# Optimization experiments

Measured on AMD Instinct MI355X. Metric: run time of the kernel, lower is better.

The kernel has to match this reference:

```python
import jax, jax.numpy as jnp
import numpy as np

N_NODES = 100000
N_EDGES = 1200000
D_IN = 64
D_OUT = 32
BN_EPS = 1e-5


def setup_inputs() -> dict:
    key = jax.random.key(0)
    ks = jax.random.split(key, 8)
    x = jax.random.normal(ks[0], (N_NODES, D_IN), dtype=jnp.float32)
    edge_index = jax.random.randint(ks[1], (2, N_EDGES), 0, N_NODES, dtype=jnp.int64)
    W1s = jax.random.normal(ks[2], (3, D_IN, D_IN), dtype=jnp.float32) * 0.05
    b1s = jax.random.normal(ks[3], (3, D_IN), dtype=jnp.float32) * 0.05
    W2s = jax.random.normal(ks[4], (3, D_IN, D_IN), dtype=jnp.float32) * 0.05
    b2s = jax.random.normal(ks[5], (3, D_IN), dtype=jnp.float32) * 0.05
    gammas = jnp.ones((3, D_IN), dtype=jnp.float32)
    betas = jnp.zeros((3, D_IN), dtype=jnp.float32)
    epss = jnp.zeros((3,), dtype=jnp.float32)  # GINConv train_eps init value 0
    lin_w = jax.random.normal(ks[6], (D_IN, D_OUT), dtype=jnp.float32) * 0.05
    lin_b = jnp.zeros((D_OUT,), dtype=jnp.float32)
    return {"x": x, "edge_index": edge_index, "W1s": W1s, "b1s": b1s,
            "W2s": W2s, "b2s": b2s, "gammas": gammas, "betas": betas,
            "epss": epss, "lin_w": lin_w, "lin_b": lin_b}


def reference(x, edge_index, W1s, b1s, W2s, b2s, gammas, betas, epss, lin_w, lin_b):
    # PyG GINConv (source_to_target): out_i = nn((1+eps)*x_i + sum_{j->i} x_j)
    src = edge_index[0]
    dst = edge_index[1]
    n = x.shape[0]
    h = x
    for i in range(3):
        agg = jax.ops.segment_sum(h[src], dst, num_segments=n)  # [N, d]
        z = (1.0 + epss[i]) * h + agg
        z = jax.nn.relu(z @ W1s[i] + b1s[i])
        z = jax.nn.relu(z @ W2s[i] + b2s[i])
        # BatchNorm1d, training mode (batch statistics, biased variance)
        mu = jnp.mean(z, axis=0)
        var = jnp.var(z, axis=0)
        z = gammas[i] * (z - mu) * jax.lax.rsqrt(var + BN_EPS) + betas[i]
        h = jax.nn.relu(z)  # F.relu after each conv
    return h @ lin_w + lin_b  # [N, D_OUT]
```

## Files before the change

### kernel.cpp

```cpp
#include <hip/hip_runtime.h>
#include <hip/hip_fp16.h>

#define NBMAX 256
#define BCAP  8192
#define CHB   3584

typedef _Float16 half8 __attribute__((ext_vector_type(8)));
typedef float f32x4 __attribute__((ext_vector_type(4)));

__device__ __forceinline__ unsigned short f2h(float f) {
    __half h = __float2half_rn(f);
    return *(unsigned short*)&h;
}

__device__ __forceinline__ int scan256(int v, int* wsum, int* woff) {
    int t = threadIdx.x, lane = t & 63, wv = t >> 6;
    int x = v;
    #pragma unroll
    for (int d = 1; d < 64; d <<= 1) {
        int y = __shfl_up(x, d, 64);
        if (lane >= d) x += y;
    }
    if (lane == 63) wsum[wv] = x;
    __syncthreads();
    if (t == 0) {
        int a = 0;
        #pragma unroll
        for (int i = 0; i < 4; ++i) { woff[i] = a; a += wsum[i]; }
    }
    __syncthreads();
    return x - v + woff[wv];
}

__global__ __launch_bounds__(256) void gin_prep(const float* __restrict__ x,
                                                unsigned short* __restrict__ o, int n16,
                                                const void* __restrict__ edge,
                                                int* __restrict__ gcount,
                                                uint2* __restrict__ ebuf,
                                                int E, int nb, int nbin) {
    if ((int)blockIdx.x >= nbin) {
        int i = (blockIdx.x - nbin) * 256 + threadIdx.x;
        if (i >= n16) return;
        float4 v = ((const float4*)x)[i];
        ushort4 u;
        u.x = f2h(v.x); u.y = f2h(v.y); u.z = f2h(v.z); u.w = f2h(v.w);
        ((ushort4*)o)[i] = u;
        return;
    }
    __shared__ int cnt[NBMAX];
    __shared__ int dlt[NBMAX];
    __shared__ int cur[NBMAX];
    __shared__ int wsum[4], woff[4];
    __shared__ int s_is64;
    __shared__ uint2 buf[CHB];
    int t = threadIdx.x;
    int beg = blockIdx.x * CHB;
    int m = E - beg; if (m > CHB) m = CHB;
    if (t < nb) cnt[t] = 0;
    if (t == 0) s_is64 = 1;
    __syncthreads();
    {
        int m2 = (E < 64) ? E : 64;
        if (t < m2 && ((const int*)edge)[2 * t + 1] != 0) s_is64 = 0;
    }
    __syncthreads();
    int is64 = s_is64;
    for (int j = t; j < m; j += 256) {
        int e = beg + j;
        int d = is64 ? (int)((const long long*)edge)[E + e] : ((const int*)edge)[E + e];
        atomicAdd(&cnt[d >> 9], 1);
    }
    __syncthreads();
    int v = (t < nb) ? cnt[t] : 0;
    int excl = scan256(v, wsum, woff);
    if (t < nb) {
        int gb = v ? atomicAdd(&gcount[t], v) : 0;
        dlt[t] = t * BCAP + gb - excl;
        cur[t] = excl;
    }
    __syncthreads();
    for (int j = t; j < m; j += 256) {
        int e = beg + j;
        int s, d;
        if (is64) {
            s = (int)((const long long*)edge)[e];
            d = (int)((const long long*)edge)[E + e];
        } else {
            s = ((const int*)edge)[e];
            d = ((const int*)edge)[E + e];
        }
        int p = atomicAdd(&cur[d >> 9], 1);
        buf[p] = make_uint2((unsigned)s, (unsigned)d);
    }
    __syncthreads();
    for (int j = t; j < m; j += 256) {
        uint2 ed = buf[j];
        ebuf[j + dlt[(int)(ed.y >> 9)]] = ed;
    }
}

__global__ __launch_bounds__(256) void gin_build(const uint2* __restrict__ ebuf,
                                                 const int* __restrict__ gcount,
                                                 int* __restrict__ rowbeg,
                                                 int* __restrict__ rowend,
                                                 int* __restrict__ col, int n) {
    __shared__ int cnt[512];
    __shared__ int off[512];
    __shared__ int wsum[4], woff[4];
    int b = blockIdx.x, t = threadIdx.x;
    int beg = b * BCAP;
    int end = beg + gcount[b];
    cnt[t] = 0; cnt[t + 256] = 0;
    __syncthreads();
    for (int j = beg + t; j < end; j += 256)
        atomicAdd(&cnt[(int)(ebuf[j].y & 511)], 1);
    __syncthreads();
    int v0 = cnt[2 * t], v1 = cnt[2 * t + 1];
    int ep = scan256(v0 + v1, wsum, woff);
    off[2 * t] = ep;
    off[2 * t + 1] = ep + v0;
    __syncthreads();
    int node0 = b * 512 + 2 * t;
    if (node0 < n) {
        rowbeg[node0] = beg + off[2 * t];
        rowend[node0] = beg + off[2 * t] + v0;
    }
    if (node0 + 1 < n) {
        rowbeg[node0 + 1] = beg + off[2 * t + 1];
        rowend[node0 + 1] = beg + off[2 * t + 1] + v1;
    }
    __syncthreads();
    for (int j = beg + t; j < end; j += 256) {
        uint2 ed = ebuf[j];
        int p = atomicAdd(&off[(int)(ed.y & 511)], 1);
        col[beg + p] = (int)ed.x;
    }
}

template <bool APPLY>
__device__ __forceinline__ void accum8(float* acc, uint4 u,
                                       const float* sc, const float* sh) {
    float v[8];
    float2 f;
    f = __half22float2(*(const __half2*)&u.x); v[0] = f.x; v[1] = f.y;
    f = __half22float2(*(const __half2*)&u.y); v[2] = f.x; v[3] = f.y;
    f = __half22float2(*(const __half2*)&u.z); v[4] = f.x; v[5] = f.y;
    f = __half22float2(*(const __half2*)&u.w); v[6] = f.x; v[7] = f.y;
    #pragma unroll
    for (int j = 0; j < 8; ++j)
        acc[j] += APPLY ? fmaxf(fmaf(v[j], sc[j], sh[j]), 0.f) : v[j];
}

template <bool APPLY>
__device__ __forceinline__ void gather_node(const unsigned short* __restrict__ zb,
                                            int r0, int r1, int ci0,
                                            const int* __restrict__ col,
                                            float e1,
                                            const float* sc, const float* sh,
                                            _Float16* __restrict__ trow,
                                            int wid, int qn, int l16) {
    int r = l16 >> 3, c = l16 & 7;
    uint4 su = make_uint4(0, 0, 0, 0);
    if (r == 0) su = *(const uint4*)(zb + (size_t)wid * 64 + 8 * c);

    float acc[8] = {0.f, 0.f, 0.f, 0.f, 0.f, 0.f, 0.f, 0.f};
    int ci = ci0;
    for (int b2 = r0; b2 < r1; b2 += 16) {
        if (b2 > r0) {
            int ce = b2 + l16;
            ci = col[ce < r1 ? ce : r1 - 1];
        }
        uint4 u[8];
        bool p[8];
        #pragma unroll
        for (int s = 0; s < 8; ++s) {
            int j = 2 * s + r;
            p[s] = (b2 + j) < r1;
            int idx = __shfl(ci, 16 * qn + j);
            if (p[s]) u[s] = *(const uint4*)(zb + (size_t)idx * 64 + 8 * c);
        }
        #pragma unroll
        for (int s = 0; s < 8; ++s)
            if (p[s]) accum8<APPLY>(acc, u[s], sc, sh);
    }
    #pragma unroll
    for (int j = 0; j < 8; ++j)
        acc[j] += __shfl_xor(acc[j], 8);
    if (r == 0) {
        float s[8];
        float2 f;
        f = __half22float2(*(const __half2*)&su.x); s[0] = f.x; s[1] = f.y;
        f = __half22float2(*(const __half2*)&su.y); s[2] = f.x; s[3] = f.y;
        f = __half22float2(*(const __half2*)&su.z); s[4] = f.x; s[5] = f.y;
        f = __half22float2(*(const __half2*)&su.w); s[6] = f.x; s[7] = f.y;
        #pragma unroll
        for (int j = 0; j < 8; ++j) {
            float v = APPLY ? fmaxf(fmaf(s[j], sc[j], sh[j]), 0.f) : s[j];
            acc[j] = fmaf(e1, v, acc[j]);
        }
        uint4 o;
        o.x = (unsigned)f2h(acc[0]) | ((unsigned)f2h(acc[1]) << 16);
        o.y = (unsigned)f2h(acc[2]) | ((unsigned)f2h(acc[3]) << 16);
        o.z = (unsigned)f2h(acc[4]) | ((unsigned)f2h(acc[5]) << 16);
        o.w = (unsigned)f2h(acc[6]) | ((unsigned)f2h(acc[7]) << 16);
        *(uint4*)(trow + 8 * c) = o;
    }
}

template <bool APPLY>
__global__ __launch_bounds__(512, 4) void gin_fused(const unsigned short* __restrict__ zb,
                                                    const int* __restrict__ rowbeg,
                                                    const int* __restrict__ rowend,
                                                    const int* __restrict__ col,
                                                    const float* __restrict__ epss,
                                                    const float* __restrict__ gammas,
                                                    const float* __restrict__ betas,
                                                    float fN,
                                                    unsigned short* __restrict__ z16,
                                                    const float* __restrict__ W1g,
                                                    const float* __restrict__ b1g,
                                                    const float* __restrict__ W2g,
                                                    const float* __restrict__ b2g,
                                                    float* __restrict__ stats,
                                                    int layer, int n) {
    __shared__ _Float16 Wt[2 * 64 * 72];
    __shared__ _Float16 Tz[128 * 72];
    __shared__ float sS[64], sQ[64];
    __shared__ float sBN[128];
    int tid = threadIdx.x;
    int base = blockIdx.x * 128;
    const float* __restrict__ W1 = W1g + layer * 4096;
    const float* __restrict__ W2 = W2g + layer * 4096;

    for (int i = tid; i < 4096; i += 512) {
        int k = i >> 6, nn = i & 63;
        Wt[nn * 72 + k]        = (_Float16)W1[i];
        Wt[4608 + nn * 72 + k] = (_Float16)W2[i];
    }
    if (tid < 64) {
        sS[tid] = 0.f; sQ[tid] = 0.f;
        if (APPLY) {
            float mu  = stats[(layer - 1) * 128 + tid] / fN;
            float var = stats[(layer - 1) * 128 + 64 + tid] / fN - mu * mu;
            float g   = gammas[(layer - 1) * 64 + tid];
            float grs = g * rsqrtf(var + 1e-5f);
            sBN[tid]      = grs;
            sBN[64 + tid] = betas[(layer - 1) * 64 + tid] - grs * mu;
        }
    }
    __syncthreads();

    int lane = tid & 63, wv = tid >> 6;
    int qn = lane >> 4;
    int l16 = lane & 15;
    int c8 = l16 & 7;
    float e1 = 1.f + epss[layer];
    float sc[8] = {1.f, 1.f, 1.f, 1.f, 1.f, 1.f, 1.f, 1.f};
    float sh[8] = {0.f, 0.f, 0.f, 0.f, 0.f, 0.f, 0.f, 0.f};
    if (APPLY) {
        *(float4*)&sc[0] = *(const float4*)&sBN[8 * c8];
        *(float4*)&sc[4] = *(const float4*)&sBN[8 * c8 + 4];
        *(float4*)&sh[0] = *(const float4*)&sBN[64 + 8 * c8];
        *(float4*)&sh[4] = *(const float4*)&sBN[64 + 8 * c8 + 4];
    }

    int wvq = wv * 4 + qn;
    int cr0, cr1, pr0, pr1;
    {
        int w0 = base + wvq;
        cr0 = 0; cr1 = 0;
        if (w0 < n) { cr0 = rowbeg[w0]; cr1 = rowend[w0]; }
        int w1 = w0 + 32;
        pr0 = 0; pr1 = 0;
        if (w1 < n) { pr0 = rowbeg[w1]; pr1 = rowend[w1]; }
    }
    int cci = 0;
    if (cr1 > cr0) { int ce = cr0 + l16; cci = col[ce < cr1 ? ce : cr1 - 1]; }
    #pragma unroll 1
    for (int p = 0; p < 4; ++p) {
        int nci = 0;
        if (pr1 > pr0) { int ce = pr0 + l16; nci = col[ce < pr1 ? ce : pr1 - 1]; }
        int fr0 = 0, fr1 = 0;
        {
            int w2 = base + (p + 2) * 32 + wvq;
            if (p < 2 && w2 < n) { fr0 = rowbeg[w2]; fr1 = rowend[w2]; }
        }
        int widl = p * 32 + wvq;
        int wid = base + widl;
        if (wid < n) {
            gather_node<APPLY>(zb, cr0, cr1, cci, col, e1, sc, sh,
                               Tz + widl * 72, wid, qn, l16);
        } else if (l16 < 8) {
            *(uint4*)(Tz + widl * 72 + 8 * c8) = make_uint4(0u, 0u, 0u, 0u);
        }
        cr0 = pr0; cr1 = pr1; cci = nci;
        pr0 = fr0; pr1 = fr1;
    }
    __syncthreads();

    int g = qn, q = l16;
    int n0 = 16 * wv + q;

    half8 tb0 = *(const half8*)&Tz[n0 * 72 + 8 * g];
    half8 tb1 = *(const half8*)&Tz[n0 * 72 + 32 + 8 * g];

    f32x4 acc[4];
    #pragma unroll
    for (int ft = 0; ft < 4; ++ft)
        acc[ft] = (f32x4){0.f, 0.f, 0.f, 0.f};

    #pragma unroll
    for (int ft = 0; ft < 4; ++ft) {
        half8 a0 = *(const half8*)&Wt[(16 * ft + q) * 72 + 8 * g];
        half8 a1 = *(const half8*)&Wt[(16 * ft + q) * 72 + 32 + 8 * g];
        acc[ft] = __builtin_amdgcn_mfma_f32_16x16x32_f16(a0, tb0, acc[ft], 0, 0, 0);
        acc[ft] = __builtin_amdgcn_mfma_f32_16x16x32_f16(a1, tb1, acc[ft], 0, 0, 0);
    }

    #pragma unroll
    for (int ft = 0; ft < 4; ++ft) {
        float4 b = *(const float4*)(b1g + layer * 64 + 16 * ft + 4 * g);
        float v0 = fmaxf(acc[ft][0] + b.x, 0.f);
        float v1 = fmaxf(acc[ft][1] + b.y, 0.f);
        float v2 = fmaxf(acc[ft][2] + b.z, 0.f);
        float v3 = fmaxf(acc[ft][3] + b.w, 0.f);
        uint2 pk;
        pk.x = (unsigned)f2h(v0) | ((unsigned)f2h(v1) << 16);
        pk.y = (unsigned)f2h(v2) | ((unsigned)f2h(v3) << 16);
        *(uint2*)&Tz[n0 * 72 + 16 * ft + 4 * g] = pk;
    }

    half8 zb0 = *(const half8*)&Tz[n0 * 72 + 8 * g];
    half8 zb1 = *(const half8*)&Tz[n0 * 72 + 32 + 8 * g];
    #pragma unroll
    for (int ft = 0; ft < 4; ++ft)
        acc[ft] = (f32x4){0.f, 0.f, 0.f, 0.f};
    #pragma unroll
    for (int ft = 0; ft < 4; ++ft) {
        half8 a0 = *(const half8*)&Wt[4608 + (16 * ft + q) * 72 + 8 * g];
        half8 a1 = *(const half8*)&Wt[4608 + (16 * ft + q) * 72 + 32 + 8 * g];
        acc[ft] = __builtin_amdgcn_mfma_f32_16x16x32_f16(a0, zb0, acc[ft], 0, 0, 0);
        acc[ft] = __builtin_amdgcn_mfma_f32_16x16x32_f16(a1, zb1, acc[ft], 0, 0, 0);
    }

    int nodeg = base + n0;
    #pragma unroll
    for (int ft = 0; ft < 4; ++ft) {
        float4 b = *(const float4*)(b2g + layer * 64 + 16 * ft + 4 * g);
        float v0 = fmaxf(acc[ft][0] + b.x, 0.f);
        float v1 = fmaxf(acc[ft][1] + b.y, 0.f);
        float v2 = fmaxf(acc[ft][2] + b.z, 0.f);
        float v3 = fmaxf(acc[ft][3] + b.w, 0.f);
        float s[4], sq[4];
        bool ok = nodeg < n;
        s[0] = ok ? v0 : 0.f; sq[0] = ok ? v0 * v0 : 0.f;
        s[1] = ok ? v1 : 0.f; sq[1] = ok ? v1 * v1 : 0.f;
        s[2] = ok ? v2 : 0.f; sq[2] = ok ? v2 * v2 : 0.f;
        s[3] = ok ? v3 : 0.f; sq[3] = ok ? v3 * v3 : 0.f;
        uint2 pk;
        pk.x = (unsigned)f2h(v0) | ((unsigned)f2h(v1) << 16);
        pk.y = (unsigned)f2h(v2) | ((unsigned)f2h(v3) << 16);
        *(uint2*)&Tz[n0 * 72 + 16 * ft + 4 * g] = pk;
        #pragma unroll
        for (int off = 1; off < 16; off <<= 1) {
            #pragma unroll
            for (int r2 = 0; r2 < 4; ++r2) {
                s[r2] += __shfl_xor(s[r2], off);
                sq[r2] += __shfl_xor(sq[r2], off);
            }
        }
        if (q == 0) {
            #pragma unroll
            for (int r2 = 0; r2 < 4; ++r2) {
                atomicAdd(&sS[16 * ft + 4 * g + r2], s[r2]);
                atomicAdd(&sQ[16 * ft + 4 * g + r2], sq[r2]);
            }
        }
    }

    #pragma unroll
    for (int t2 = 0; t2 < 2; ++t2) {
        int u = lane + 64 * t2;
        int rloc = 16 * wv + (u >> 3);
        int node = base + rloc;
        if (node < n) {
            uint4 v = *(const uint4*)&Tz[rloc * 72 + (u & 7) * 8];
            *(uint4*)(z16 + (size_t)node * 64 + (u & 7) * 8) = v;
        }
    }

    __syncthreads();
    if (tid < 64) {
        atomicAdd(&stats[layer * 128 + tid], sS[tid]);
        atomicAdd(&stats[layer * 128 + 64 + tid], sQ[tid]);
    }
}

__global__ __launch_bounds__(256) void gin_lin(const unsigned short* __restrict__ zin,
                                               const float* __restrict__ stats,
                                               const float* __restrict__ gammas,
                                               const float* __restrict__ betas,
                                               float fN,
                                               const float* __restrict__ lw,
                                               const float* __restrict__ lb,
                                               float* __restrict__ out, int n) {
    __shared__ float Z[128 * 68];
    int tid = threadIdx.x;
    int base = blockIdx.x * 128;
    int cq = (tid & 15) * 4;
    float4 sc4, sh4;
    {
        float t0[4], t1[4];
        #pragma unroll
        for (int j = 0; j < 4; ++j) {
            int f = cq + j;
            float mu  = stats[256 + f] / fN;
            float var = stats[256 + 64 + f] / fN - mu * mu;
            float g   = gammas[128 + f];
            float grs = g * rsqrtf(var + 1e-5f);
            t0[j] = grs;
            t1[j] = betas[128 + f] - grs * mu;
        }
        sc4 = make_float4(t0[0], t0[1], t0[2], t0[3]);
        sh4 = make_float4(t1[0], t1[1], t1[2], t1[3]);
    }
    {
        const ushort4* __restrict__ src = (const ushort4*)(zin + (size_t)base * 64);
        #pragma unroll
        for (int it = 0; it < 8; ++it) {
            int idx4 = it * 256 + tid;
            int row = idx4 >> 4, c = (idx4 & 15) * 4;
            float4 v = make_float4(0.f, 0.f, 0.f, 0.f);
            if (base + row < n) {
                ushort4 u = src[idx4];
                float2 f0 = __half22float2(*(const __half2*)&u.x);
                float2 f1 = __half22float2(*(const __half2*)&u.z);
                v = make_float4(f0.x, f0.y, f1.x, f1.y);
            }
            float4 r;
            r.x = fmaxf(fmaf(v.x, sc4.x, sh4.x), 0.f);
            r.y = fmaxf(fmaf(v.y, sc4.y, sh4.y), 0.f);
            r.z = fmaxf(fmaf(v.z, sc4.z, sh4.z), 0.f);
            r.w = fmaxf(fmaf(v.w, sc4.w, sh4.w), 0.f);
            *(float4*)&Z[row * 68 + c] = r;
        }
    }
    __syncthreads();
    int tx = tid & 7, ty = tid >> 3;
    float acc[4][4];
    {
        float4 b = *(const float4*)(lb + 4 * tx);
        #pragma unroll
        for (int r = 0; r < 4; ++r) {
            acc[r][0] = b.x; acc[r][1] = b.y; acc[r][2] = b.z; acc[r][3] = b.w;
        }
    }
    #pragma unroll 4
    for (int k = 0; k < 64; ++k) {
        float4 w = *(const float4*)(lw + k * 32 + 4 * tx);
        #pragma unroll
        for (int r = 0; r < 4; ++r) {
            float a = Z[(ty + 32 * r) * 68 + k];
            acc[r][0] = fmaf(a, w.x, acc[r][0]);
            acc[r][1] = fmaf(a, w.y, acc[r][1]);
            acc[r][2] = fmaf(a, w.z, acc[r][2]);
            acc[r][3] = fmaf(a, w.w, acc[r][3]);
        }
    }
    #pragma unroll
    for (int r = 0; r < 4; ++r) {
        int row = base + ty + 32 * r;
        if (row < n) {
            float4 v;
            v.x = acc[r][0]; v.y = acc[r][1]; v.z = acc[r][2]; v.w = acc[r][3];
            *(float4*)(out + (size_t)row * 32 + 4 * tx) = v;
        }
    }
}

extern "C" void kernel_launch(void* const* d_in, const int* in_sizes, int n_in,
                              void* d_out, int out_size, void* d_ws, size_t ws_size,
                              hipStream_t stream) {
    const float* x      = (const float*)d_in[0];
    const void*  edge   = d_in[1];
    const float* W1s    = (const float*)d_in[2];
    const float* b1s    = (const float*)d_in[3];
    const float* W2s    = (const float*)d_in[4];
    const float* b2s    = (const float*)d_in[5];
    const float* gammas = (const float*)d_in[6];
    const float* betas  = (const float*)d_in[7];
    const float* epss   = (const float*)d_in[8];
    const float* lin_w  = (const float*)d_in[9];
    const float* lin_b  = (const float*)d_in[10];
    float* out = (float*)d_out;

    const int N = in_sizes[0] / 64;
    const int E = in_sizes[1] / 2;
    const int NB = (N + 511) >> 9;
    const float fN = (float)N;

    char* w = (char*)d_ws;
    auto take = [&](size_t bytes) {
        char* p = w;
        w += (bytes + 255) & ~(size_t)255;
        return p;
    };
    unsigned short* x16 = (unsigned short*)take((size_t)N * 64 * 2);
    unsigned short* hA  = (unsigned short*)take((size_t)N * 64 * 2);
    unsigned short* hB  = (unsigned short*)take((size_t)N * 64 * 2);
    uint2* ebuf    = (uint2*)take((size_t)NB * BCAP * 8);
    int*   col     = (int*)take((size_t)NB * BCAP * 4);
    int*   rowbeg  = (int*)take((size_t)N * 4);
    int*   rowend  = (int*)take((size_t)N * 4);
    int*   gcount  = (int*)take((size_t)NBMAX * 4);
    float* stats   = (float*)take(3 * 128 * 4);

    hipMemsetAsync(gcount, 0, 1024 + 1536, stream);

    const int n16 = N * 16;
    const int nbin = (E + CHB - 1) / CHB;
    const int gx = (n16 + 255) / 256;
    gin_prep<<<nbin + gx, 256, 0, stream>>>(x, x16, n16, edge, gcount, ebuf, E, NB, nbin);
    gin_build<<<NB, 256, 0, stream>>>(ebuf, gcount, rowbeg, rowend, col, N);

    const int gMlp = (N + 127) / 128;
    const unsigned short* zin = x16;
    unsigned short* zout = hA;
    for (int L = 0; L < 3; ++L) {
        if (L == 0)
            gin_fused<false><<<gMlp, 512, 0, stream>>>(zin, rowbeg, rowend, col, epss,
                                                       gammas, betas, fN, zout,
                                                       W1s, b1s, W2s, b2s, stats, L, N);
        else
            gin_fused<true><<<gMlp, 512, 0, stream>>>(zin, rowbeg, rowend, col, epss,
                                                      gammas, betas, fN, zout,
                                                      W1s, b1s, W2s, b2s, stats, L, N);
        zin = zout;
        zout = (zout == hA) ? hB : hA;
    }
    gin_lin<<<gMlp, 256, 0, stream>>>(zin, stats, gammas, betas, fN, lin_w, lin_b, out, N);
}
```

Before: 301.9 us.

## Fuse final linear layer into last GIN layer via cooperative grid sync

The third GIN layer's kernel becomes a cooperative launch. Each block publishes its BatchNorm partial sums, waits on a grid-wide sync for the global statistics, then applies BN, ReLU and the final 64x32 linear projection to its 128-row tile still held in shared memory. This removes the fp16 write of the last hidden state, its re-read by the separate gin_lin kernel, and one launch. In exchange every block must be co-resident, and there are extra host-side occupancy queries on each call; if the cooperative launch is not possible, the code falls back to the old two-kernel path.

```diff
diff --git a/kernel.cpp b/kernel.cpp
--- a/kernel.cpp
+++ b/kernel.cpp
@@ -1,5 +1,6 @@
 #include <hip/hip_runtime.h>
 #include <hip/hip_fp16.h>
+#include <hip/hip_cooperative_groups.h>
 
 #define NBMAX 256
 #define BCAP  8192
@@ -207,7 +208,7 @@
     }
 }
 
-template <bool APPLY>
+template <bool APPLY, bool FINAL>
 __global__ __launch_bounds__(512, 4) void gin_fused(const unsigned short* __restrict__ zb,
                                                     const int* __restrict__ rowbeg,
                                                     const int* __restrict__ rowend,
@@ -222,7 +223,10 @@
                                                     const float* __restrict__ W2g,
                                                     const float* __restrict__ b2g,
                                                     float* __restrict__ stats,
-                                                    int layer, int n) {
+                                                    int layer, int n,
+                                                    const float* __restrict__ lw,
+                                                    const float* __restrict__ lb,
+                                                    float* __restrict__ out) {
     __shared__ _Float16 Wt[2 * 64 * 72];
     __shared__ _Float16 Tz[128 * 72];
     __shared__ float sS[64], sQ[64];
@@ -378,21 +382,76 @@
         }
     }
 
-    #pragma unroll
-    for (int t2 = 0; t2 < 2; ++t2) {
-        int u = lane + 64 * t2;
-        int rloc = 16 * wv + (u >> 3);
-        int node = base + rloc;
-        if (node < n) {
-            uint4 v = *(const uint4*)&Tz[rloc * 72 + (u & 7) * 8];
-            *(uint4*)(z16 + (size_t)node * 64 + (u & 7) * 8) = v;
-        }
-    }
-
-    __syncthreads();
-    if (tid < 64) {
-        atomicAdd(&stats[layer * 128 + tid], sS[tid]);
-        atomicAdd(&stats[layer * 128 + 64 + tid], sQ[tid]);
+    if constexpr (!FINAL) {
+        #pragma unroll
+        for (int t2 = 0; t2 < 2; ++t2) {
+            int u = lane + 64 * t2;
+            int rloc = 16 * wv + (u >> 3);
+            int node = base + rloc;
+            if (node < n) {
+                uint4 v = *(const uint4*)&Tz[rloc * 72 + (u & 7) * 8];
+                *(uint4*)(z16 + (size_t)node * 64 + (u & 7) * 8) = v;
+            }
+        }
+        __syncthreads();
+        if (tid < 64) {
+            atomicAdd(&stats[layer * 128 + tid], sS[tid]);
+            atomicAdd(&stats[layer * 128 + 64 + tid], sQ[tid]);
+        }
+    } else {
+        __syncthreads();
+        if (tid < 64) {
+            atomicAdd(&stats[layer * 128 + tid], sS[tid]);
+            atomicAdd(&stats[layer * 128 + 64 + tid], sQ[tid]);
+        }
+        __threadfence();
+        cooperative_groups::this_grid().sync();
+
+        float* Wl = (float*)Wt;
+        for (int i = tid; i < 2048; i += 512) Wl[i] = lw[i];
+        if (tid < 64) {
+            float mu  = stats[layer * 128 + tid] / fN;
+            float var = stats[layer * 128 + 64 + tid] / fN - mu * mu;
+            float g2  = gammas[layer * 64 + tid];
+            float grs = g2 * rsqrtf(var + 1e-5f);
+            sBN[tid]      = grs;
+            sBN[64 + tid] = betas[layer * 64 + tid] - grs * mu;
+        }
+        __syncthreads();
+
+        int tx = tid & 7, ty = tid >> 3;
+        float accL[2][4];
+        {
+            float4 b = *(const float4*)(lb + 4 * tx);
+            #pragma unroll
+            for (int r = 0; r < 2; ++r) {
+                accL[r][0] = b.x; accL[r][1] = b.y; accL[r][2] = b.z; accL[r][3] = b.w;
+            }
+        }
+        #pragma unroll 4
+        for (int k = 0; k < 64; ++k) {
+            float4 w2 = *(const float4*)&Wl[k * 32 + 4 * tx];
+            float s_ = sBN[k], h_ = sBN[64 + k];
+            #pragma unroll
+            for (int r = 0; r < 2; ++r) {
+                int row = ty + 64 * r;
+                float zv = (float)Tz[row * 72 + k];
+                float a = fmaxf(fmaf(zv, s_, h_), 0.f);
+                accL[r][0] = fmaf(a, w2.x, accL[r][0]);
+                accL[r][1] = fmaf(a, w2.y, accL[r][1]);
+                accL[r][2] = fmaf(a, w2.z, accL[r][2]);
+                accL[r][3] = fmaf(a, w2.w, accL[r][3]);
+            }
+        }
+        #pragma unroll
+        for (int r = 0; r < 2; ++r) {
+            int row = base + ty + 64 * r;
+            if (row < n) {
+                float4 v;
+                v.x = accL[r][0]; v.y = accL[r][1]; v.z = accL[r][2]; v.w = accL[r][3];
+                *(float4*)(out + (size_t)row * 32 + 4 * tx) = v;
+            }
+        }
     }
 }
 
@@ -524,19 +583,50 @@
     gin_build<<<NB, 256, 0, stream>>>(ebuf, gcount, rowbeg, rowend, col, N);
 
     const int gMlp = (N + 127) / 128;
-    const unsigned short* zin = x16;
-    unsigned short* zout = hA;
-    for (int L = 0; L < 3; ++L) {
-        if (L == 0)
-            gin_fused<false><<<gMlp, 512, 0, stream>>>(zin, rowbeg, rowend, col, epss,
-                                                       gammas, betas, fN, zout,
-                                                       W1s, b1s, W2s, b2s, stats, L, N);
-        else
-            gin_fused<true><<<gMlp, 512, 0, stream>>>(zin, rowbeg, rowend, col, epss,
-                                                      gammas, betas, fN, zout,
-                                                      W1s, b1s, W2s, b2s, stats, L, N);
-        zin = zout;
-        zout = (zout == hA) ? hB : hA;
-    }
-    gin_lin<<<gMlp, 256, 0, stream>>>(zin, stats, gammas, betas, fN, lin_w, lin_b, out, N);
-}
+
+    gin_fused<false, false><<<gMlp, 512, 0, stream>>>(x16, rowbeg, rowend, col, epss,
+                                                      gammas, betas, fN, hA,
+                                                      W1s, b1s, W2s, b2s, stats, 0, N,
+                                                      nullptr, nullptr, nullptr);
+    gin_fused<true, false><<<gMlp, 512, 0, stream>>>(hA, rowbeg, rowend, col, epss,
+                                                     gammas, betas, fN, hB,
+                                                     W1s, b1s, W2s, b2s, stats, 1, N,
+                                                     nullptr, nullptr, nullptr);
+
+    bool coop = false;
+    {
+        int dev = 0;
+        hipGetDevice(&dev);
+        int numCU = 0;
+        hipDeviceGetAttribute(&numCU, hipDeviceAttributeMultiprocessorCount, dev);
+        int maxB = 0;
+        hipOccupancyMaxActiveBlocksPerMultiprocessor(
+            &maxB, reinterpret_cast<const void*>(&gin_fused<true, true>), 512, 0);
+        if (maxB > 0 && numCU > 0 && (long long)maxB * numCU >= (long long)gMlp)
+            coop = true;
+    }
+    if (coop) {
+        const unsigned short* zi = hB;
+        unsigned short* zo = hA;
+        int Lv = 2, Nv = N;
+        float fNv = fN;
+        void* args[] = {
+            (void*)&zi, (void*)&rowbeg, (void*)&rowend, (void*)&col,
+            (void*)&epss, (void*)&gammas, (void*)&betas, (void*)&fNv,
+            (void*)&zo, (void*)&W1s, (void*)&b1s, (void*)&W2s, (void*)&b2s,
+            (void*)&stats, (void*)&Lv, (void*)&Nv,
+            (void*)&lin_w, (void*)&lin_b, (void*)&out
+        };
+        hipError_t err = hipLaunchCooperativeKernel(
+            reinterpret_cast<const void*>(&gin_fused<true, true>),
+            dim3(gMlp), dim3(512), args, 0, stream);
+        if (err != hipSuccess) coop = false;
+    }
+    if (!coop) {
+        gin_fused<true, false><<<gMlp, 512, 0, stream>>>(hB, rowbeg, rowend, col, epss,
+                                                         gammas, betas, fN, hA,
+                                                         W1s, b1s, W2s, b2s, stats, 2, N,
+                                                         nullptr, nullptr, nullptr);
+        gin_lin<<<gMlp, 256, 0, stream>>>(hA, stats, gammas, betas, fN, lin_w, lin_b, out, N);
+    }
+}
```

After: 301.2 us. No clear change (-0.2%).
